# Optimization experiments

Measured on AMD Instinct MI355X. Metric: run time of the kernel, lower is better.

## Reference

```python
import jax, jax.numpy as jnp
import numpy as np

NUM_USERS = 100000
NUM_ITEMS = 50000
EMBED_DIM = 64
N_LAYERS = 3
N_EDGES = 2400000
N_NODES = NUM_USERS + NUM_ITEMS


def setup_inputs() -> dict:
    key = jax.random.key(0)
    k1, k2, k3 = jax.random.split(key, 3)
    # Xavier-uniform init for embedding tables
    bound_u = float(np.sqrt(6.0 / (NUM_USERS + EMBED_DIM)))
    bound_i = float(np.sqrt(6.0 / (NUM_ITEMS + EMBED_DIM)))
    user_emb = jax.random.uniform(k1, (NUM_USERS, EMBED_DIM), jnp.float32, -bound_u, bound_u)
    item_emb = jax.random.uniform(k2, (NUM_ITEMS, EMBED_DIM), jnp.float32, -bound_i, bound_i)
    edge_index = jax.random.randint(k3, (2, N_EDGES), 0, N_NODES, dtype=jnp.int32)
    return {"user_emb": user_emb, "item_emb": item_emb, "edge_index": edge_index}


def _propagate(x, row, col):
    # degree-normalized gather-scale-scatter: out[row] += x[col] * rsqrt(deg[row]*deg[col])
    n = x.shape[0]
    deg = jnp.clip(jnp.zeros((n,), x.dtype).at[row].add(1.0), 1.0)  # bincount, clamp(min=1)
    norm = jax.lax.rsqrt(deg[row]) * jax.lax.rsqrt(deg[col])        # [E]
    return jnp.zeros_like(x).at[row].add(x[col] * norm[:, None])   # scatter-add [N,d]


def reference(user_emb, item_emb, edge_index):
    row, col = edge_index[0], edge_index[1]
    all_emb = jnp.concatenate([user_emb, item_emb], axis=0)  # [N, d]
    acc = all_emb
    x = all_emb
    for _ in range(N_LAYERS):
        x = _propagate(x, row, col)
        acc = acc + x
    final_emb = acc / (N_LAYERS + 1)  # mean over layer-0..n_layers embeddings
    return final_emb[:NUM_USERS], final_emb[NUM_USERS:]
```

## Files before the change

### kernel.cpp

```cpp
#include <hip/hip_runtime.h>


#define NUM_USERS 100000
#define NUM_ITEMS 50000
#define EMBED_DIM 64
#define N_NODES   150000
#define N_EDGES   2400000
#define N_BUCKETS 586
#define BCAP      4608
#define PART_BLOCKS 256

#define OFF_BCNT 0
#define OFF_BE   8192
#define OFF_RSQD 1208192
#define OFF_PS   1808256
#define OFF_XA   12611584
#define OFF_XB   31813632

__device__ __forceinline__ unsigned f2bf(float f) {
    unsigned u = __float_as_uint(f);
    return (u + 0x7fffu + ((u >> 16) & 1u)) >> 16;
}
__device__ __forceinline__ float bflo(unsigned u) { return __uint_as_float(u << 16); }
__device__ __forceinline__ float bfhi(unsigned u) { return __uint_as_float(u & 0xffff0000u); }
__device__ __forceinline__ float2 bf2(unsigned u) {
    float2 r; r.x = bflo(u); r.y = bfhi(u); return r;
}

__global__ void partition_kernel(const int4* __restrict__ row4, const int4* __restrict__ col4,
                                 int* __restrict__ bcnt, unsigned* __restrict__ ps,
                                 uint2* __restrict__ yA, uint2* __restrict__ yB) {
    __shared__ int lh[N_BUCKETS];
    if (blockIdx.x == 0 && threadIdx.x < 16) {
        uint2 z; z.x = 0u; z.y = 0u;
        yA[2400000 + threadIdx.x] = z;
        yB[2400000 + threadIdx.x] = z;
    }
    for (int t = threadIdx.x; t < N_BUCKETS; t += blockDim.x) lh[t] = 0;
    __syncthreads();
    const int total4 = N_EDGES / 4;
    int per4 = (total4 + gridDim.x - 1) / gridDim.x;
    int s4 = blockIdx.x * per4;
    int e4 = s4 + per4; if (e4 > total4) e4 = total4;
    for (int i = s4 + (int)threadIdx.x; i < e4; i += (int)blockDim.x) {
        int4 r = row4[i];
        atomicAdd(&lh[r.x >> 8], 1);
        atomicAdd(&lh[r.y >> 8], 1);
        atomicAdd(&lh[r.z >> 8], 1);
        atomicAdd(&lh[r.w >> 8], 1);
    }
    __syncthreads();
    for (int t = threadIdx.x; t < N_BUCKETS; t += blockDim.x) {
        int c = lh[t];
        lh[t] = c ? (t * BCAP + atomicAdd(&bcnt[t], c)) : 0;
    }
    __syncthreads();
    for (int i = s4 + (int)threadIdx.x; i < e4; i += (int)blockDim.x) {
        int4 r = row4[i];
        int4 c = col4[i];
        int pos;
        pos = atomicAdd(&lh[r.x >> 8], 1); ps[pos] = ((unsigned)(r.x & 255) << 18) | (unsigned)c.x;
        pos = atomicAdd(&lh[r.y >> 8], 1); ps[pos] = ((unsigned)(r.y & 255) << 18) | (unsigned)c.y;
        pos = atomicAdd(&lh[r.z >> 8], 1); ps[pos] = ((unsigned)(r.z & 255) << 18) | (unsigned)c.z;
        pos = atomicAdd(&lh[r.w >> 8], 1); ps[pos] = ((unsigned)(r.w & 255) << 18) | (unsigned)c.w;
    }
}

__global__ void fine_kernel(const int* __restrict__ bcnt, int* __restrict__ ps,
                            int2* __restrict__ be, float* __restrict__ rsqd,
                            const float4* __restrict__ user, const float4* __restrict__ item,
                            uint2* __restrict__ yA) {
    __shared__ int ledge[BCAP];
    __shared__ int rh[256];
    __shared__ int rsc[256];
    __shared__ int rcur[256];
    __shared__ float rq[256];
    int b = blockIdx.x;
    int base = b * BCAP;
    int cnt  = bcnt[b];
    if (cnt > BCAP) cnt = BCAP;
    rh[threadIdx.x] = 0;
    __syncthreads();
    for (int i = threadIdx.x; i < cnt; i += 256) {
        int p = ps[base + i];
        ledge[i] = p;
        atomicAdd(&rh[p >> 18], 1);
    }
    __syncthreads();
    rsc[threadIdx.x] = (rh[threadIdx.x] + 1) & ~1;
    __syncthreads();
    for (int off = 1; off < 256; off <<= 1) {
        int t = (threadIdx.x >= off) ? rsc[threadIdx.x - off] : 0;
        __syncthreads();
        rsc[threadIdx.x] += t;
        __syncthreads();
    }
    {
        int r = threadIdx.x;
        int sz = (rh[r] + 1) & ~1;
        int pstart = rsc[r] - sz;
        rcur[r] = pstart;
        int n = (b << 8) + r;
        if (n < N_NODES) {
            int2 p; p.x = base + pstart; p.y = base + pstart + rh[r];
            be[n] = p;
            float d = (float)(rh[r] < 1 ? 1 : rh[r]);
            float rn = rsqrtf(d);
            rq[r] = rn;
            rsqd[n] = rn;
        }
    }
    __syncthreads();
    for (int i = threadIdx.x; i < cnt; i += 256) {
        int p = ledge[i];
        int pos = atomicAdd(&rcur[p >> 18], 1);
        ps[base + pos] = p & 0x3FFFF;
    }
    for (int idx = threadIdx.x; idx < 4096; idx += 256) {
        int r = idx >> 4, w = idx & 15;
        int n = (b << 8) + r;
        if (n < N_NODES) {
            const float4* src = (n < NUM_USERS) ? (user + (size_t)n * 16)
                                                : (item + (size_t)(n - NUM_USERS) * 16);
            float4 v = src[w];
            float rn = rq[r];
            uint2 o;
            o.x = f2bf(v.x * rn) | (f2bf(v.y * rn) << 16);
            o.y = f2bf(v.z * rn) | (f2bf(v.w * rn) << 16);
            yA[(size_t)n * 16 + w] = o;
        }
    }
}

__device__ __forceinline__ void pull_body(int n, int lane, const int2* be,
                                          const int2* scol2, const uint4* xin, float2 sum[4]) {
    int g = lane >> 3;
    int q = lane & 7;
    int2 bnd = be[n];
    int j = bnd.x, endj = bnd.y;
    for (; j < endj; j += 16) {
        int p0 = j + 2 * g;
        int2 cc = scol2[p0 >> 1];
        int c0 = (p0     < endj) ? cc.x : N_NODES;
        int c1 = (p0 + 1 < endj) ? cc.y : N_NODES;
        uint4 X0 = xin[(size_t)c0 * 8 + q];
        uint4 X1 = xin[(size_t)c1 * 8 + q];
        sum[0] += bf2(X0.x) + bf2(X1.x);
        sum[1] += bf2(X0.y) + bf2(X1.y);
        sum[2] += bf2(X0.z) + bf2(X1.z);
        sum[3] += bf2(X0.w) + bf2(X1.w);
    }
#pragma unroll
    for (int off = 8; off < 64; off <<= 1) {
#pragma unroll
        for (int k = 0; k < 4; ++k) {
            sum[k].x += __shfl_xor(sum[k].x, off);
            sum[k].y += __shfl_xor(sum[k].y, off);
        }
    }
}

__global__ void pull_kernel(const int2* __restrict__ be,
                            const int2* __restrict__ scol2, const float* __restrict__ rsqd,
                            const uint4* __restrict__ xin, uint4* __restrict__ xout) {
    int n = blockIdx.x * 4 + ((int)threadIdx.x >> 6);
    if (n >= N_NODES) return;
    int lane = threadIdx.x & 63;
    float2 sum[4];
    sum[0] = make_float2(0.f, 0.f); sum[1] = make_float2(0.f, 0.f);
    sum[2] = make_float2(0.f, 0.f); sum[3] = make_float2(0.f, 0.f);
    pull_body(n, lane, be, scol2, xin, sum);
    if ((lane >> 3) == 0) {
        int q = lane & 7;
        float rn = rsqd[n];
        float s2 = rn * rn;
        uint4 p;
        p.x = f2bf(sum[0].x * s2) | (f2bf(sum[0].y * s2) << 16);
        p.y = f2bf(sum[1].x * s2) | (f2bf(sum[1].y * s2) << 16);
        p.z = f2bf(sum[2].x * s2) | (f2bf(sum[2].y * s2) << 16);
        p.w = f2bf(sum[3].x * s2) | (f2bf(sum[3].y * s2) << 16);
        xout[(size_t)n * 8 + q] = p;
    }
}

__global__ void pull_last_kernel(const int2* __restrict__ be,
                                 const int2* __restrict__ scol2, const float* __restrict__ rsqd,
                                 const uint4* __restrict__ xin,
                                 const uint4* __restrict__ xprev,
                                 const float4* __restrict__ user, const float4* __restrict__ item,
                                 float4* __restrict__ acc4) {
    int n = blockIdx.x * 4 + ((int)threadIdx.x >> 6);
    if (n >= N_NODES) return;
    int lane = threadIdx.x & 63;
    float2 sum[4];
    sum[0] = make_float2(0.f, 0.f); sum[1] = make_float2(0.f, 0.f);
    sum[2] = make_float2(0.f, 0.f); sum[3] = make_float2(0.f, 0.f);
    pull_body(n, lane, be, scol2, xin, sum);
    if ((lane >> 3) == 0) {
        int q = lane & 7;
        float rn = rsqd[n];
        float sd = 1.0f / rn;
        uint4 p2 = xin  [(size_t)n * 8 + q];
        uint4 p1 = xprev[(size_t)n * 8 + q];
        const float4* x0 = (n < NUM_USERS) ? (user + (size_t)n * 16)
                                           : (item + (size_t)(n - NUM_USERS) * 16);
        float4 a0 = x0[q * 2], a1 = x0[q * 2 + 1];
        float4 o0, o1;
        o0.x = (a0.x + (bflo(p1.x) + bflo(p2.x)) * sd + rn * sum[0].x) * 0.25f;
        o0.y = (a0.y + (bfhi(p1.x) + bfhi(p2.x)) * sd + rn * sum[0].y) * 0.25f;
        o0.z = (a0.z + (bflo(p1.y) + bflo(p2.y)) * sd + rn * sum[1].x) * 0.25f;
        o0.w = (a0.w + (bfhi(p1.y) + bfhi(p2.y)) * sd + rn * sum[1].y) * 0.25f;
        o1.x = (a1.x + (bflo(p1.z) + bflo(p2.z)) * sd + rn * sum[2].x) * 0.25f;
        o1.y = (a1.y + (bfhi(p1.z) + bfhi(p2.z)) * sd + rn * sum[2].y) * 0.25f;
        o1.z = (a1.z + (bflo(p1.w) + bflo(p2.w)) * sd + rn * sum[3].x) * 0.25f;
        o1.w = (a1.w + (bfhi(p1.w) + bfhi(p2.w)) * sd + rn * sum[3].y) * 0.25f;
        size_t o4 = (size_t)n * 16 + q * 2;
        acc4[o4] = o0;
        acc4[o4 + 1] = o1;
    }
}

extern "C" void kernel_launch(void* const* d_in, const int* in_sizes, int n_in,
                              void* d_out, int out_size, void* d_ws, size_t ws_size,
                              hipStream_t stream) {
    const float* user = (const float*)d_in[0];
    const float* item = (const float*)d_in[1];
    const int*   ei   = (const int*)d_in[2];
    const int* row = ei;
    const int* col = ei + N_EDGES;

    char*  ws   = (char*)d_ws;
    int*   bcnt = (int*)(ws + OFF_BCNT);
    int2*  be   = (int2*)(ws + OFF_BE);
    float* rsqd = (float*)(ws + OFF_RSQD);
    int*   ps   = (int*)(ws + OFF_PS);
    char*  xA   = ws + OFF_XA;
    char*  xB   = ws + OFF_XB;
    float* acc  = (float*)d_out;

    hipMemsetAsync(bcnt, 0, N_BUCKETS * sizeof(int), stream);
    partition_kernel<<<PART_BLOCKS, 1024, 0, stream>>>((const int4*)row, (const int4*)col,
                                                       bcnt, (unsigned*)ps,
                                                       (uint2*)xA, (uint2*)xB);
    fine_kernel<<<N_BUCKETS, 256, 0, stream>>>(bcnt, ps, be, rsqd,
                                               (const float4*)user, (const float4*)item,
                                               (uint2*)xA);

    const int grid = (N_NODES + 3) / 4;
    pull_kernel<<<grid, 256, 0, stream>>>(be, (const int2*)ps, rsqd,
        (const uint4*)xA, (uint4*)xB);
    pull_kernel<<<grid, 256, 0, stream>>>(be, (const int2*)ps, rsqd,
        (const uint4*)xB, (uint4*)xA);
    pull_last_kernel<<<grid, 256, 0, stream>>>(be, (const int2*)ps, rsqd,
        (const uint4*)xA, (const uint4*)xB,
        (const float4*)user, (const float4*)item, (float4*)acc);
}
```

Baseline: 323.7 us.

## Assign eight lanes per node in pull kernels instead of a full wavefront

Each node's pull is now handled by an 8-lane group that walks its whole neighbor list serially, two edges per step, in place of a 64-lane wavefront split into 8 edge groups followed by a shuffle reduction. This removes the cross-lane shuffle reduction and the idle lanes on low-degree nodes (average degree is about 16), and gives 8x more active nodes per wavefront. The trade-off is longer serial loops per lane and divergence inside a wavefront when degrees differ across the 8 nodes it covers.

Measured after the change: 296.7 us. -8.3%, faster.

```diff
diff --git a/kernel.cpp b/kernel.cpp
--- a/kernel.cpp
+++ b/kernel.cpp
@@ -132,17 +132,15 @@
     }
 }
 
-__device__ __forceinline__ void pull_body(int n, int lane, const int2* be,
-                                          const int2* scol2, const uint4* xin, float2 sum[4]) {
-    int g = lane >> 3;
-    int q = lane & 7;
+__device__ __forceinline__ void pull_sum(int n, int q, const int2* __restrict__ be,
+                                         const int2* __restrict__ scol2,
+                                         const uint4* __restrict__ xin, float2 sum[4]) {
     int2 bnd = be[n];
-    int j = bnd.x, endj = bnd.y;
-    for (; j < endj; j += 16) {
-        int p0 = j + 2 * g;
-        int2 cc = scol2[p0 >> 1];
-        int c0 = (p0     < endj) ? cc.x : N_NODES;
-        int c1 = (p0 + 1 < endj) ? cc.y : N_NODES;
+    int endj = bnd.y;
+    for (int j = bnd.x; j < endj; j += 2) {
+        int2 cc = scol2[j >> 1];
+        int c0 = cc.x;
+        int c1 = (j + 1 < endj) ? cc.y : N_NODES;
         uint4 X0 = xin[(size_t)c0 * 8 + q];
         uint4 X1 = xin[(size_t)c1 * 8 + q];
         sum[0] += bf2(X0.x) + bf2(X1.x);
@@ -150,37 +148,27 @@
         sum[2] += bf2(X0.z) + bf2(X1.z);
         sum[3] += bf2(X0.w) + bf2(X1.w);
     }
-#pragma unroll
-    for (int off = 8; off < 64; off <<= 1) {
-#pragma unroll
-        for (int k = 0; k < 4; ++k) {
-            sum[k].x += __shfl_xor(sum[k].x, off);
-            sum[k].y += __shfl_xor(sum[k].y, off);
-        }
-    }
 }
 
 __global__ void pull_kernel(const int2* __restrict__ be,
                             const int2* __restrict__ scol2, const float* __restrict__ rsqd,
                             const uint4* __restrict__ xin, uint4* __restrict__ xout) {
-    int n = blockIdx.x * 4 + ((int)threadIdx.x >> 6);
+    int t = blockIdx.x * blockDim.x + (int)threadIdx.x;
+    int n = t >> 3;
     if (n >= N_NODES) return;
-    int lane = threadIdx.x & 63;
+    int q = t & 7;
     float2 sum[4];
     sum[0] = make_float2(0.f, 0.f); sum[1] = make_float2(0.f, 0.f);
     sum[2] = make_float2(0.f, 0.f); sum[3] = make_float2(0.f, 0.f);
-    pull_body(n, lane, be, scol2, xin, sum);
-    if ((lane >> 3) == 0) {
-        int q = lane & 7;
-        float rn = rsqd[n];
-        float s2 = rn * rn;
-        uint4 p;
-        p.x = f2bf(sum[0].x * s2) | (f2bf(sum[0].y * s2) << 16);
-        p.y = f2bf(sum[1].x * s2) | (f2bf(sum[1].y * s2) << 16);
-        p.z = f2bf(sum[2].x * s2) | (f2bf(sum[2].y * s2) << 16);
-        p.w = f2bf(sum[3].x * s2) | (f2bf(sum[3].y * s2) << 16);
-        xout[(size_t)n * 8 + q] = p;
-    }
+    pull_sum(n, q, be, scol2, xin, sum);
+    float rn = rsqd[n];
+    float s2 = rn * rn;
+    uint4 p;
+    p.x = f2bf(sum[0].x * s2) | (f2bf(sum[0].y * s2) << 16);
+    p.y = f2bf(sum[1].x * s2) | (f2bf(sum[1].y * s2) << 16);
+    p.z = f2bf(sum[2].x * s2) | (f2bf(sum[2].y * s2) << 16);
+    p.w = f2bf(sum[3].x * s2) | (f2bf(sum[3].y * s2) << 16);
+    xout[(size_t)n * 8 + q] = p;
 }
 
 __global__ void pull_last_kernel(const int2* __restrict__ be,
@@ -189,35 +177,33 @@
                                  const uint4* __restrict__ xprev,
                                  const float4* __restrict__ user, const float4* __restrict__ item,
                                  float4* __restrict__ acc4) {
-    int n = blockIdx.x * 4 + ((int)threadIdx.x >> 6);
+    int t = blockIdx.x * blockDim.x + (int)threadIdx.x;
+    int n = t >> 3;
     if (n >= N_NODES) return;
-    int lane = threadIdx.x & 63;
+    int q = t & 7;
     float2 sum[4];
     sum[0] = make_float2(0.f, 0.f); sum[1] = make_float2(0.f, 0.f);
     sum[2] = make_float2(0.f, 0.f); sum[3] = make_float2(0.f, 0.f);
-    pull_body(n, lane, be, scol2, xin, sum);
-    if ((lane >> 3) == 0) {
-        int q = lane & 7;
-        float rn = rsqd[n];
-        float sd = 1.0f / rn;
-        uint4 p2 = xin  [(size_t)n * 8 + q];
-        uint4 p1 = xprev[(size_t)n * 8 + q];
-        const float4* x0 = (n < NUM_USERS) ? (user + (size_t)n * 16)
-                                           : (item + (size_t)(n - NUM_USERS) * 16);
-        float4 a0 = x0[q * 2], a1 = x0[q * 2 + 1];
-        float4 o0, o1;
-        o0.x = (a0.x + (bflo(p1.x) + bflo(p2.x)) * sd + rn * sum[0].x) * 0.25f;
-        o0.y = (a0.y + (bfhi(p1.x) + bfhi(p2.x)) * sd + rn * sum[0].y) * 0.25f;
-        o0.z = (a0.z + (bflo(p1.y) + bflo(p2.y)) * sd + rn * sum[1].x) * 0.25f;
-        o0.w = (a0.w + (bfhi(p1.y) + bfhi(p2.y)) * sd + rn * sum[1].y) * 0.25f;
-        o1.x = (a1.x + (bflo(p1.z) + bflo(p2.z)) * sd + rn * sum[2].x) * 0.25f;
-        o1.y = (a1.y + (bfhi(p1.z) + bfhi(p2.z)) * sd + rn * sum[2].y) * 0.25f;
-        o1.z = (a1.z + (bflo(p1.w) + bflo(p2.w)) * sd + rn * sum[3].x) * 0.25f;
-        o1.w = (a1.w + (bfhi(p1.w) + bfhi(p2.w)) * sd + rn * sum[3].y) * 0.25f;
-        size_t o4 = (size_t)n * 16 + q * 2;
-        acc4[o4] = o0;
-        acc4[o4 + 1] = o1;
-    }
+    pull_sum(n, q, be, scol2, xin, sum);
+    float rn = rsqd[n];
+    float sd = 1.0f / rn;
+    uint4 p2 = xin  [(size_t)n * 8 + q];
+    uint4 p1 = xprev[(size_t)n * 8 + q];
+    const float4* x0 = (n < NUM_USERS) ? (user + (size_t)n * 16)
+                                       : (item + (size_t)(n - NUM_USERS) * 16);
+    float4 a0 = x0[q * 2], a1 = x0[q * 2 + 1];
+    float4 o0, o1;
+    o0.x = (a0.x + (bflo(p1.x) + bflo(p2.x)) * sd + rn * sum[0].x) * 0.25f;
+    o0.y = (a0.y + (bfhi(p1.x) + bfhi(p2.x)) * sd + rn * sum[0].y) * 0.25f;
+    o0.z = (a0.z + (bflo(p1.y) + bflo(p2.y)) * sd + rn * sum[1].x) * 0.25f;
+    o0.w = (a0.w + (bfhi(p1.y) + bfhi(p2.y)) * sd + rn * sum[1].y) * 0.25f;
+    o1.x = (a1.x + (bflo(p1.z) + bflo(p2.z)) * sd + rn * sum[2].x) * 0.25f;
+    o1.y = (a1.y + (bfhi(p1.z) + bfhi(p2.z)) * sd + rn * sum[2].y) * 0.25f;
+    o1.z = (a1.z + (bflo(p1.w) + bflo(p2.w)) * sd + rn * sum[3].x) * 0.25f;
+    o1.w = (a1.w + (bfhi(p1.w) + bfhi(p2.w)) * sd + rn * sum[3].y) * 0.25f;
+    size_t o4 = (size_t)n * 16 + q * 2;
+    acc4[o4] = o0;
+    acc4[o4 + 1] = o1;
 }
 
 extern "C" void kernel_launch(void* const* d_in, const int* in_sizes, int n_in,
@@ -246,7 +232,7 @@
                                                (const float4*)user, (const float4*)item,
                                                (uint2*)xA);
 
-    const int grid = (N_NODES + 3) / 4;
+    const int grid = (N_NODES * 8 + 255) / 256;
     pull_kernel<<<grid, 256, 0, stream>>>(be, (const int2*)ps, rsqd,
         (const uint4*)xA, (uint4*)xB);
     pull_kernel<<<grid, 256, 0, stream>>>(be, (const int2*)ps, rsqd,
```
